# Optimization experiments

Measured on AMD Instinct MI355X. Metric: run time of the kernel, lower is better.

Reference implementation:

```python
import jax, jax.numpy as jnp
import numpy as np

ROPE_THETA = 10000.0
N_KV_HEADS = 8


def _rope(x, pos, theta):
    # x: [..., D] with interleaved (even, odd) rotation pairs; pos: scalar position
    D = x.shape[-1]
    freqs = theta ** (-jnp.arange(0, D, 2, dtype=jnp.float32) / D)  # [D/2]
    ang = pos * freqs
    cos, sin = jnp.cos(ang), jnp.sin(ang)
    x1, x2 = x[..., 0::2], x[..., 1::2]
    return jnp.stack([x1 * cos - x2 * sin, x1 * sin + x2 * cos], axis=-1).reshape(x.shape)


def setup_inputs() -> dict:
    key = jax.random.key(0)
    ks = jax.random.split(key, 5)
    B, DIM, CACHE_LEN, HD = 32, 4096, 4096, 128
    N_HEADS = 32
    qkv_out = (N_HEADS + 2 * N_KV_HEADS) * HD  # 6144
    return {
        "x": jax.random.normal(ks[0], (B, DIM), dtype=jnp.float32),
        "cache_k": jax.random.normal(ks[1], (B, CACHE_LEN, N_KV_HEADS, HD), dtype=jnp.float32),
        "cache_v": jax.random.normal(ks[2], (B, CACHE_LEN, N_KV_HEADS, HD), dtype=jnp.float32),
        "wqkv": jax.random.normal(ks[3], (qkv_out, DIM), dtype=jnp.float32) * 0.02,
        "wo": jax.random.normal(ks[4], (DIM, DIM), dtype=jnp.float32) * 0.02,
        "ctx_len": 4095,
    }


def reference(x, cache_k, cache_v, wqkv, wo, ctx_len):
    B = x.shape[0]
    n_kv = cache_k.shape[2]
    hd = cache_k.shape[3]
    n_heads = (wqkv.shape[0] - 2 * n_kv * hd) // hd
    hpg = n_heads // n_kv  # heads per kv group

    # fused QKV projection
    xqkv = x @ wqkv.T  # [B, (n_heads + 2*n_kv)*hd]
    nq = n_heads * hd
    nk = n_kv * hd
    q = xqkv[:, :nq].reshape(B, n_kv, hpg, hd)
    k = xqkv[:, nq:nq + nk].reshape(B, n_kv, hd)
    v = xqkv[:, nq + nk:].reshape(B, n_kv, hd)

    # rope fused with KV-cache write: new token at position ctx_len
    q = _rope(q, ctx_len, ROPE_THETA)
    k = _rope(k, ctx_len, ROPE_THETA)
    cache_k = cache_k.at[:, ctx_len].set(k)
    cache_v = cache_v.at[:, ctx_len].set(v)

    T = ctx_len + 1  # valid cache length (python int -> static slice)
    K = cache_k[:, :T]  # [B, T, n_kv, hd]
    V = cache_v[:, :T]

    # GQA attention: q [b, g, h, d], K/V [b, t, g, d]
    scores = jnp.einsum("bghd,btgd->bght", q, K) / jnp.sqrt(jnp.float32(hd))
    w = jax.nn.softmax(scores, axis=-1)
    o = jnp.einsum("bght,btgd->bghd", w, V).reshape(B, n_heads * hd)
    return o @ wo.T
```

## Files before the change

kernel.cpp:

```cpp
#include <hip/hip_runtime.h>
#include <math.h>

#define BATCH 32
#define DIM   4096
#define CLEN  4096
#define HD    128
#define NKV   8
#define NHEAD 32
#define QKVN  6144
#define GN    64
#define KSEG  128
#define KSTG  4
#define KTOT  512
#define NSEG  8
#define NCH   16
#define TC    256
#define NSLOT 32
#define MNEG  -1.0e30f

template <int CTRL>
__device__ __forceinline__ float dpp_add(float x) {
  int y = __builtin_amdgcn_update_dpp(0, __float_as_int(x), CTRL, 0xF, 0xF, true);
  return x + __int_as_float(y);
}

__device__ __forceinline__ float half_reduce(float s) {
  s = dpp_add<0xB1>(s);
  s = dpp_add<0x4E>(s);
  s = dpp_add<0x124>(s);
  s = dpp_add<0x128>(s);
  s += __int_as_float(__builtin_amdgcn_ds_swizzle(__float_as_int(s), 0x401F));
  return s;
}

__global__ __launch_bounds__(256)
void gemm_partial(const float* __restrict__ X, const float* __restrict__ W,
                  float* __restrict__ part, const int N) {
  __shared__ float xs[KSEG][BATCH + 4];
  __shared__ float wl[KSEG][GN + 4];
  const int tid = threadIdx.x;
  const int n0  = blockIdx.x * GN;
  const int k00 = blockIdx.y * KTOT;
  const int c = tid & 31;
  const int r = tid >> 5;
  const int bq = (tid & 7) << 2;
  const int nq = (tid >> 3) << 1;
  float a00=0,a01=0, a10=0,a11=0, a20=0,a21=0, a30=0,a31=0;

  for (int kk = 0; kk < KSTG; ++kk) {
    const int k0 = k00 + kk * KSEG;
    if (kk) __syncthreads();
#pragma unroll
    for (int p = 0; p < 4; ++p) {
      const int b = p * 8 + r;
      const float4 v = *(const float4*)(X + (size_t)b * DIM + k0 + c * 4);
      const int k = c * 4;
      xs[k][b] = v.x; xs[k + 1][b] = v.y; xs[k + 2][b] = v.z; xs[k + 3][b] = v.w;
    }
#pragma unroll
    for (int p = 0; p < 8; ++p) {
      const int n = p * 8 + r;
      const float4 v = *(const float4*)(W + (size_t)(n0 + n) * DIM + k0 + c * 4);
      const int k = c * 4;
      wl[k][n] = v.x; wl[k + 1][n] = v.y; wl[k + 2][n] = v.z; wl[k + 3][n] = v.w;
    }
    __syncthreads();
#pragma unroll 8
    for (int k = 0; k < KSEG; ++k) {
      const float4 xv = *(const float4*)&xs[k][bq];
      const float2 wv = *(const float2*)&wl[k][nq];
      a00 += xv.x * wv.x; a01 += xv.x * wv.y;
      a10 += xv.y * wv.x; a11 += xv.y * wv.y;
      a20 += xv.z * wv.x; a21 += xv.z * wv.y;
      a30 += xv.w * wv.x; a31 += xv.w * wv.y;
    }
  }
  float* base = part + ((size_t)blockIdx.y * BATCH + bq) * N + n0 + nq;
  *(float2*)(base)         = make_float2(a00, a01);
  *(float2*)(base + N)     = make_float2(a10, a11);
  *(float2*)(base + 2 * N) = make_float2(a20, a21);
  *(float2*)(base + 3 * N) = make_float2(a30, a31);
}

__global__ __launch_bounds__(256)
void qkv_combine(const float* __restrict__ part, const int* __restrict__ ctxp,
                 float* __restrict__ qw, float* __restrict__ kn, float* __restrict__ vn) {
  const int idx = blockIdx.x * 256 + threadIdx.x;
  const int b  = idx / (QKVN / 2);
  const int c  = idx % (QKVN / 2);
  const int n0 = c * 2;
  float v0 = 0.f, v1 = 0.f;
#pragma unroll
  for (int s = 0; s < NSEG; ++s) {
    const float2 pv = *(const float2*)(part + ((size_t)s * BATCH + b) * QKVN + n0);
    v0 += pv.x; v1 += pv.y;
  }
  const float pos = (float)ctxp[0];
  const float L2T_OVER_64 = 0.20762050593045952f;
  if (n0 < DIM) {
    const int i = (n0 & 127) >> 1;
    const float fr = exp2f(-(float)i * L2T_OVER_64);
    float sn, cs; sincosf(pos * fr, &sn, &cs);
    qw[(size_t)b * DIM + n0]     = v0 * cs - v1 * sn;
    qw[(size_t)b * DIM + n0 + 1] = v0 * sn + v1 * cs;
  } else if (n0 < DIM + NKV * HD) {
    const int nk = n0 - DIM;
    const int i = (nk & 127) >> 1;
    const float fr = exp2f(-(float)i * L2T_OVER_64);
    float sn, cs; sincosf(pos * fr, &sn, &cs);
    kn[(size_t)b * (NKV * HD) + nk]     = v0 * cs - v1 * sn;
    kn[(size_t)b * (NKV * HD) + nk + 1] = v0 * sn + v1 * cs;
  } else {
    const int nv = n0 - DIM - NKV * HD;
    vn[(size_t)b * (NKV * HD) + nv]     = v0;
    vn[(size_t)b * (NKV * HD) + nv + 1] = v1;
  }
}

__global__ __launch_bounds__(256, 4)
void attn_fd(const float* __restrict__ qw, const float* __restrict__ knew,
             const float* __restrict__ vnew, const float* __restrict__ ck,
             const float* __restrict__ cv, const int* __restrict__ ctxp,
             float* __restrict__ opart, float* __restrict__ mlp) {
  const int bg   = blockIdx.x;
  const int b = bg >> 3, g = bg & 7;
  const int wid  = threadIdx.x >> 6;
  const int lane = threadIdx.x & 63;
  const int half = lane >> 5;
  const int d4   = (lane & 31) << 2;
  const int cidx = blockIdx.y * 4 + wid;
  const int T    = ctxp[0] + 1;
  const int ctx  = T - 1;
  const int c0   = cidx * TC;

  const float sc = 0.08838834764831845f;
  float4 q[4];
#pragma unroll
  for (int hh = 0; hh < 4; ++hh) {
    q[hh] = *(const float4*)(qw + ((size_t)b * NHEAD + g * 4 + hh) * HD + d4);
    q[hh].x *= sc; q[hh].y *= sc; q[hh].z *= sc; q[hh].w *= sc;
  }
  const float* ckb = ck + ((size_t)b * CLEN * NKV + g) * HD + d4;
  const float* cvb = cv + ((size_t)b * CLEN * NKV + g) * HD + d4;
  const float* knr = knew + ((size_t)b * NKV + g) * HD + d4;
  const float* vnr = vnew + ((size_t)b * NKV + g) * HD + d4;

  float m[4] = {MNEG, MNEG, MNEG, MNEG};
  float l[4] = {0.f, 0.f, 0.f, 0.f};
  float4 acc[4] = {};

  for (int it = 0; it < TC / 8; ++it) {
    const int t0 = c0 + it * 8;
    float4 kb[4], vb[4];
#pragma unroll
    for (int u = 0; u < 4; ++u) {
      const int tr = t0 + u * 2 + half;
      const float* kp = (tr == ctx) ? knr : (ckb + (size_t)tr * (NKV * HD));
      const float* vp = (tr == ctx) ? vnr : (cvb + (size_t)tr * (NKV * HD));
      kb[u] = *(const float4*)kp;
      vb[u] = *(const float4*)vp;
    }
#pragma unroll
    for (int u = 0; u < 4; ++u) {
      const int tr = t0 + u * 2 + half;
      float s[4];
#pragma unroll
      for (int hh = 0; hh < 4; ++hh) {
        float d = kb[u].x * q[hh].x + kb[u].y * q[hh].y
                + kb[u].z * q[hh].z + kb[u].w * q[hh].w;
        s[hh] = half_reduce(d);
      }
      if (tr >= T) { s[0] = MNEG * 2.f; s[1] = MNEG * 2.f; s[2] = MNEG * 2.f; s[3] = MNEG * 2.f; }
      const bool grow = (s[0] > m[0]) | (s[1] > m[1]) | (s[2] > m[2]) | (s[3] > m[3]);
      if (grow) {
#pragma unroll
        for (int hh = 0; hh < 4; ++hh) {
          const float mn = fmaxf(m[hh], s[hh]);
          const float rs = __expf(m[hh] - mn);
          l[hh] *= rs;
          acc[hh].x *= rs; acc[hh].y *= rs; acc[hh].z *= rs; acc[hh].w *= rs;
          m[hh] = mn;
        }
      }
#pragma unroll
      for (int hh = 0; hh < 4; ++hh) {
        const float p = __expf(s[hh] - m[hh]);
        l[hh] += p;
        acc[hh].x += p * vb[u].x; acc[hh].y += p * vb[u].y;
        acc[hh].z += p * vb[u].z; acc[hh].w += p * vb[u].w;
      }
    }
  }

#pragma unroll
  for (int hh = 0; hh < 4; ++hh) {
    const int hid = b * NHEAD + g * 4 + hh;
    const size_t slot = (size_t)hid * NSLOT + cidx * 2 + half;
    *(float4*)(opart + slot * HD + d4) = acc[hh];
    if ((lane & 31) == 0) { mlp[slot * 2] = m[hh]; mlp[slot * 2 + 1] = l[hh]; }
  }
}

__global__ __launch_bounds__(128)
void attn_combine(const float* __restrict__ opart, const float* __restrict__ mlp,
                  float* __restrict__ ow) {
  const int p = blockIdx.x;
  const int d = threadIdx.x;
  float M = MNEG;
#pragma unroll
  for (int c = 0; c < NSLOT; ++c) M = fmaxf(M, mlp[((size_t)p * NSLOT + c) * 2]);
  float L = 0.f, O = 0.f;
#pragma unroll 8
  for (int c = 0; c < NSLOT; ++c) {
    const float mi = mlp[((size_t)p * NSLOT + c) * 2];
    const float w = __expf(mi - M);
    L += w * mlp[((size_t)p * NSLOT + c) * 2 + 1];
    O += w * opart[((size_t)p * NSLOT + c) * HD + d];
  }
  ow[(size_t)p * HD + d] = O / L;
}

__global__ __launch_bounds__(256)
void sum_partials(const float* __restrict__ part, float* __restrict__ out,
                  const int total4, const int nseg, const int stride) {
  const int i = blockIdx.x * 256 + threadIdx.x;
  if (i >= total4) return;
  float4 s = make_float4(0.f, 0.f, 0.f, 0.f);
  for (int g = 0; g < nseg; ++g) {
    const float4 v = *(const float4*)(part + (size_t)g * stride + (size_t)i * 4);
    s.x += v.x; s.y += v.y; s.z += v.z; s.w += v.w;
  }
  *(float4*)(out + (size_t)i * 4) = s;
}

extern "C" void kernel_launch(void* const* d_in, const int* in_sizes, int n_in,
                              void* d_out, int out_size, void* d_ws, size_t ws_size,
                              hipStream_t stream) {
  const float* x    = (const float*)d_in[0];
  const float* ck   = (const float*)d_in[1];
  const float* cv   = (const float*)d_in[2];
  const float* wqkv = (const float*)d_in[3];
  const float* wo   = (const float*)d_in[4];
  const int*   ctx  = (const int*)d_in[5];

  float* ws    = (float*)d_ws;
  float* pqkv  = ws;
  float* qw    = pqkv + (size_t)NSEG * BATCH * QKVN;
  float* kn    = qw + (size_t)BATCH * DIM;
  float* vn    = kn + (size_t)BATCH * NKV * HD;
  float* opart = vn + (size_t)BATCH * NKV * HD;
  float* mlp   = opart + (size_t)1024 * NSLOT * HD;
  float* ow    = mlp + (size_t)1024 * NSLOT * 2;
  float* pout  = pqkv;

  gemm_partial<<<dim3(QKVN / GN, NSEG), 256, 0, stream>>>(x, wqkv, pqkv, QKVN);
  qkv_combine<<<dim3(BATCH * QKVN / 2 / 256), 256, 0, stream>>>(pqkv, ctx, qw, kn, vn);
  attn_fd<<<dim3(BATCH * NKV, NCH / 4), 256, 0, stream>>>(qw, kn, vn, ck, cv, ctx, opart, mlp);
  attn_combine<<<dim3(BATCH * NHEAD), HD, 0, stream>>>(opart, mlp, ow);
  gemm_partial<<<dim3(DIM / GN, NSEG), 256, 0, stream>>>(ow, wo, pout, DIM);
  sum_partials<<<dim3((BATCH * DIM / 4 + 255) / 256), 256, 0, stream>>>(
      pout, (float*)d_out, BATCH * DIM / 4, NSEG, BATCH * DIM);
}
```

Measured before the change: 309.9 us.

## Swizzle GEMM LDS layout, double-buffer KV loads, merge half-wave partials in attention

```diff
diff --git a/kernel.cpp b/kernel.cpp
--- a/kernel.cpp
+++ b/kernel.cpp
@@ -8,6 +8,7 @@
 #define NKV   8
 #define NHEAD 32
 #define QKVN  6144
+#define KVSTR (NKV * HD)
 #define GN    64
 #define KSEG  128
 #define KSTG  4
@@ -15,8 +16,9 @@
 #define NSEG  8
 #define NCH   16
 #define TC    256
-#define NSLOT 32
+#define NSLOT 16
 #define MNEG  -1.0e30f
+#define SMASK -3.0e38f
 
 template <int CTRL>
 __device__ __forceinline__ float dpp_add(float x) {
@@ -33,48 +35,84 @@
   return s;
 }
 
+__device__ __forceinline__ float xhalf32(float v, int lane) {
+  return __int_as_float(__builtin_amdgcn_ds_bpermute((lane ^ 32) << 2, __float_as_int(v)));
+}
+
 __global__ __launch_bounds__(256)
 void gemm_partial(const float* __restrict__ X, const float* __restrict__ W,
                   float* __restrict__ part, const int N) {
-  __shared__ float xs[KSEG][BATCH + 4];
-  __shared__ float wl[KSEG][GN + 4];
+  __shared__ float xs[KSEG * 32];
+  __shared__ float wl[KSEG * 64];
   const int tid = threadIdx.x;
+  const int c   = tid & 31;
+  const int r   = tid >> 5;
+  const int cx7 = c & 7;
   const int n0  = blockIdx.x * GN;
   const int k00 = blockIdx.y * KTOT;
-  const int c = tid & 31;
-  const int r = tid >> 5;
-  const int bq = (tid & 7) << 2;
-  const int nq = (tid >> 3) << 1;
+  const int bq8 = tid & 7;
+  const int tq  = tid >> 3;
+  const int nqq = tq >> 1;
+  const int nqo = (tq & 1) << 1;
+
   float a00=0,a01=0, a10=0,a11=0, a20=0,a21=0, a30=0,a31=0;
+
+  float* xwp  = xs + (c * 4) * 32 + ((r ^ cx7) << 2);
+  float* wwp0 = wl + (c * 4) * 64 + ((r ^ cx7) << 2);
+  float* wwp1 = wwp0 + 32;
 
   for (int kk = 0; kk < KSTG; ++kk) {
     const int k0 = k00 + kk * KSEG;
+    const float* Xp = X + (size_t)(r * 4) * DIM + k0 + c * 4;
+    const float4 xv0 = *(const float4*)(Xp);
+    const float4 xv1 = *(const float4*)(Xp + DIM);
+    const float4 xv2 = *(const float4*)(Xp + 2 * DIM);
+    const float4 xv3 = *(const float4*)(Xp + 3 * DIM);
+    const float* Wp0 = W + (size_t)(n0 + r * 4) * DIM + k0 + c * 4;
+    const float4 wv00 = *(const float4*)(Wp0);
+    const float4 wv01 = *(const float4*)(Wp0 + DIM);
+    const float4 wv02 = *(const float4*)(Wp0 + 2 * DIM);
+    const float4 wv03 = *(const float4*)(Wp0 + 3 * DIM);
+    const float* Wp1 = Wp0 + (size_t)32 * DIM;
+    const float4 wv10 = *(const float4*)(Wp1);
+    const float4 wv11 = *(const float4*)(Wp1 + DIM);
+    const float4 wv12 = *(const float4*)(Wp1 + 2 * DIM);
+    const float4 wv13 = *(const float4*)(Wp1 + 3 * DIM);
+
     if (kk) __syncthreads();
-#pragma unroll
-    for (int p = 0; p < 4; ++p) {
-      const int b = p * 8 + r;
-      const float4 v = *(const float4*)(X + (size_t)b * DIM + k0 + c * 4);
-      const int k = c * 4;
-      xs[k][b] = v.x; xs[k + 1][b] = v.y; xs[k + 2][b] = v.z; xs[k + 3][b] = v.w;
-    }
-#pragma unroll
-    for (int p = 0; p < 8; ++p) {
-      const int n = p * 8 + r;
-      const float4 v = *(const float4*)(W + (size_t)(n0 + n) * DIM + k0 + c * 4);
-      const int k = c * 4;
-      wl[k][n] = v.x; wl[k + 1][n] = v.y; wl[k + 2][n] = v.z; wl[k + 3][n] = v.w;
-    }
+
+    *(float4*)(xwp + 0)   = make_float4(xv0.x, xv1.x, xv2.x, xv3.x);
+    *(float4*)(xwp + 32)  = make_float4(xv0.y, xv1.y, xv2.y, xv3.y);
+    *(float4*)(xwp + 64)  = make_float4(xv0.z, xv1.z, xv2.z, xv3.z);
+    *(float4*)(xwp + 96)  = make_float4(xv0.w, xv1.w, xv2.w, xv3.w);
+    *(float4*)(wwp0 + 0)   = make_float4(wv00.x, wv01.x, wv02.x, wv03.x);
+    *(float4*)(wwp0 + 64)  = make_float4(wv00.y, wv01.y, wv02.y, wv03.y);
+    *(float4*)(wwp0 + 128) = make_float4(wv00.z, wv01.z, wv02.z, wv03.z);
+    *(float4*)(wwp0 + 192) = make_float4(wv00.w, wv01.w, wv02.w, wv03.w);
+    *(float4*)(wwp1 + 0)   = make_float4(wv10.x, wv11.x, wv12.x, wv13.x);
+    *(float4*)(wwp1 + 64)  = make_float4(wv10.y, wv11.y, wv12.y, wv13.y);
+    *(float4*)(wwp1 + 128) = make_float4(wv10.z, wv11.z, wv12.z, wv13.z);
+    *(float4*)(wwp1 + 192) = make_float4(wv10.w, wv11.w, wv12.w, wv13.w);
     __syncthreads();
+
 #pragma unroll 8
-    for (int k = 0; k < KSEG; ++k) {
-      const float4 xv = *(const float4*)&xs[k][bq];
-      const float2 wv = *(const float2*)&wl[k][nq];
-      a00 += xv.x * wv.x; a01 += xv.x * wv.y;
-      a10 += xv.y * wv.x; a11 += xv.y * wv.y;
-      a20 += xv.z * wv.x; a21 += xv.z * wv.y;
-      a30 += xv.w * wv.x; a31 += xv.w * wv.y;
-    }
-  }
+    for (int k2 = 0; k2 < KSEG / 4; ++k2) {
+      const int g = k2 & 7;
+      const float* xr = xs + (k2 * 4) * 32 + ((bq8 ^ g) << 2);
+      const float* wr = wl + (k2 * 4) * 64 + ((nqq ^ g) << 2) + nqo;
+#pragma unroll
+      for (int j = 0; j < 4; ++j) {
+        const float4 xv = *(const float4*)(xr + j * 32);
+        const float2 wv = *(const float2*)(wr + j * 64);
+        a00 = fmaf(xv.x, wv.x, a00); a01 = fmaf(xv.x, wv.y, a01);
+        a10 = fmaf(xv.y, wv.x, a10); a11 = fmaf(xv.y, wv.y, a11);
+        a20 = fmaf(xv.z, wv.x, a20); a21 = fmaf(xv.z, wv.y, a21);
+        a30 = fmaf(xv.w, wv.x, a30); a31 = fmaf(xv.w, wv.y, a31);
+      }
+    }
+  }
+  const int bq = bq8 << 2;
+  const int nq = tq << 1;
   float* base = part + ((size_t)blockIdx.y * BATCH + bq) * N + n0 + nq;
   *(float2*)(base)         = make_float2(a00, a01);
   *(float2*)(base + N)     = make_float2(a10, a11);
@@ -117,7 +155,63 @@
   }
 }
 
-__global__ __launch_bounds__(256, 4)
+__device__ __forceinline__ void load8(float4 kb[4], float4 vb[4],
+    const float* __restrict__ ckb, const float* __restrict__ cvb,
+    const float* __restrict__ knr, const float* __restrict__ vnr,
+    const int t0, const int half, const int ctx, const bool edge) {
+#pragma unroll
+  for (int u = 0; u < 4; ++u) {
+    const int tr = t0 + u * 2 + half;
+    const float* kp = ckb + (size_t)tr * KVSTR;
+    const float* vp = cvb + (size_t)tr * KVSTR;
+    if (edge) {
+      if (tr == ctx) { kp = knr; vp = vnr; }
+    }
+    kb[u] = *(const float4*)kp;
+    vb[u] = *(const float4*)vp;
+  }
+}
+
+__device__ __forceinline__ void compute8(const float4 kb[4], const float4 vb[4],
+    const float4 q[4], const int t0, const int half, const int ctx, const bool edge,
+    float m[4], float l[4], float4 acc[4]) {
+#pragma unroll
+  for (int u = 0; u < 4; ++u) {
+    float s[4];
+#pragma unroll
+    for (int hh = 0; hh < 4; ++hh) {
+      float d = fmaf(kb[u].x, q[hh].x, kb[u].y * q[hh].y);
+      d = fmaf(kb[u].z, q[hh].z, d);
+      d = fmaf(kb[u].w, q[hh].w, d);
+      s[hh] = half_reduce(d);
+    }
+    if (edge) {
+      const int tr = t0 + u * 2 + half;
+      if (tr > ctx) { s[0] = SMASK; s[1] = SMASK; s[2] = SMASK; s[3] = SMASK; }
+    }
+    if ((s[0] > m[0]) | (s[1] > m[1]) | (s[2] > m[2]) | (s[3] > m[3])) {
+#pragma unroll
+      for (int hh = 0; hh < 4; ++hh) {
+        const float mn = fmaxf(m[hh], s[hh]);
+        const float rs = __expf(m[hh] - mn);
+        l[hh] *= rs;
+        acc[hh].x *= rs; acc[hh].y *= rs; acc[hh].z *= rs; acc[hh].w *= rs;
+        m[hh] = mn;
+      }
+    }
+#pragma unroll
+    for (int hh = 0; hh < 4; ++hh) {
+      const float p = __expf(s[hh] - m[hh]);
+      l[hh] += p;
+      acc[hh].x = fmaf(p, vb[u].x, acc[hh].x);
+      acc[hh].y = fmaf(p, vb[u].y, acc[hh].y);
+      acc[hh].z = fmaf(p, vb[u].z, acc[hh].z);
+      acc[hh].w = fmaf(p, vb[u].w, acc[hh].w);
+    }
+  }
+}
+
+__global__ __launch_bounds__(256)
 void attn_fd(const float* __restrict__ qw, const float* __restrict__ knew,
              const float* __restrict__ vnew, const float* __restrict__ ck,
              const float* __restrict__ cv, const int* __restrict__ ctxp,
@@ -129,8 +223,7 @@
   const int half = lane >> 5;
   const int d4   = (lane & 31) << 2;
   const int cidx = blockIdx.y * 4 + wid;
-  const int T    = ctxp[0] + 1;
-  const int ctx  = T - 1;
+  const int ctx  = ctxp[0];
   const int c0   = cidx * TC;
 
   const float sc = 0.08838834764831845f;
@@ -149,55 +242,45 @@
   float l[4] = {0.f, 0.f, 0.f, 0.f};
   float4 acc[4] = {};
 
-  for (int it = 0; it < TC / 8; ++it) {
-    const int t0 = c0 + it * 8;
-    float4 kb[4], vb[4];
-#pragma unroll
-    for (int u = 0; u < 4; ++u) {
-      const int tr = t0 + u * 2 + half;
-      const float* kp = (tr == ctx) ? knr : (ckb + (size_t)tr * (NKV * HD));
-      const float* vp = (tr == ctx) ? vnr : (cvb + (size_t)tr * (NKV * HD));
-      kb[u] = *(const float4*)kp;
-      vb[u] = *(const float4*)vp;
-    }
-#pragma unroll
-    for (int u = 0; u < 4; ++u) {
-      const int tr = t0 + u * 2 + half;
-      float s[4];
-#pragma unroll
-      for (int hh = 0; hh < 4; ++hh) {
-        float d = kb[u].x * q[hh].x + kb[u].y * q[hh].y
-                + kb[u].z * q[hh].z + kb[u].w * q[hh].w;
-        s[hh] = half_reduce(d);
-      }
-      if (tr >= T) { s[0] = MNEG * 2.f; s[1] = MNEG * 2.f; s[2] = MNEG * 2.f; s[3] = MNEG * 2.f; }
-      const bool grow = (s[0] > m[0]) | (s[1] > m[1]) | (s[2] > m[2]) | (s[3] > m[3]);
-      if (grow) {
-#pragma unroll
-        for (int hh = 0; hh < 4; ++hh) {
-          const float mn = fmaxf(m[hh], s[hh]);
-          const float rs = __expf(m[hh] - mn);
-          l[hh] *= rs;
-          acc[hh].x *= rs; acc[hh].y *= rs; acc[hh].z *= rs; acc[hh].w *= rs;
-          m[hh] = mn;
-        }
-      }
-#pragma unroll
-      for (int hh = 0; hh < 4; ++hh) {
-        const float p = __expf(s[hh] - m[hh]);
-        l[hh] += p;
-        acc[hh].x += p * vb[u].x; acc[hh].y += p * vb[u].y;
-        acc[hh].z += p * vb[u].z; acc[hh].w += p * vb[u].w;
-      }
-    }
+  float4 ka[4], va[4], kb2[4], vb2[4];
+  int t = c0;
+  load8(ka, va, ckb, cvb, knr, vnr, t, half, ctx, t + 8 > ctx);
+  for (int it = 0; it < TC / 16; ++it) {
+    const int tb = t + 8;
+    load8(kb2, vb2, ckb, cvb, knr, vnr, tb, half, ctx, tb + 8 > ctx);
+    compute8(ka, va, q, t, half, ctx, t + 8 > ctx, m, l, acc);
+    const int tn = t + 16;
+    if (it + 1 < TC / 16)
+      load8(ka, va, ckb, cvb, knr, vnr, tn, half, ctx, tn + 8 > ctx);
+    compute8(kb2, vb2, q, tb, half, ctx, tb + 8 > ctx, m, l, acc);
+    t = tn;
   }
 
 #pragma unroll
   for (int hh = 0; hh < 4; ++hh) {
-    const int hid = b * NHEAD + g * 4 + hh;
-    const size_t slot = (size_t)hid * NSLOT + cidx * 2 + half;
-    *(float4*)(opart + slot * HD + d4) = acc[hh];
-    if ((lane & 31) == 0) { mlp[slot * 2] = m[hh]; mlp[slot * 2 + 1] = l[hh]; }
+    const float mo = xhalf32(m[hh], lane);
+    const float lo = xhalf32(l[hh], lane);
+    float4 ao;
+    ao.x = xhalf32(acc[hh].x, lane); ao.y = xhalf32(acc[hh].y, lane);
+    ao.z = xhalf32(acc[hh].z, lane); ao.w = xhalf32(acc[hh].w, lane);
+    const float mc = fmaxf(m[hh], mo);
+    const float wa = __expf(m[hh] - mc);
+    const float wb = __expf(mo - mc);
+    l[hh] = wa * l[hh] + wb * lo;
+    acc[hh].x = wa * acc[hh].x + wb * ao.x;
+    acc[hh].y = wa * acc[hh].y + wb * ao.y;
+    acc[hh].z = wa * acc[hh].z + wb * ao.z;
+    acc[hh].w = wa * acc[hh].w + wb * ao.w;
+    m[hh] = mc;
+  }
+  if (half == 0) {
+#pragma unroll
+    for (int hh = 0; hh < 4; ++hh) {
+      const int hid = b * NHEAD + g * 4 + hh;
+      const size_t slot = (size_t)hid * NSLOT + cidx;
+      *(float4*)(opart + slot * HD + d4) = acc[hh];
+      if ((lane & 31) == 0) { mlp[slot * 2] = m[hh]; mlp[slot * 2 + 1] = l[hh]; }
+    }
   }
 }
 
```

Result: faster. 269.7 us (-13.0%).
